# Optimization experiments

Measured on AMD Instinct MI355X. Metric: run time of the kernel, lower is better.

Reference implementation:

```python
import jax, jax.numpy as jnp
import numpy as np

B, D, H = 512, 256, 512

def setup_inputs() -> dict:
    key = jax.random.key(0)
    ks = jax.random.split(key, 7)
    s = lambda fan_in: 1.0 / np.sqrt(fan_in)
    return {
        "h": jax.random.normal(ks[0], (B, D), jnp.float32),
        "W1": jax.random.normal(ks[1], (2 * D, H), jnp.float32) * s(2 * D),
        "b1": jax.random.normal(ks[2], (H,), jnp.float32) * s(2 * D),
        "W2": jax.random.normal(ks[3], (H, H), jnp.float32) * s(H),
        "b2": jax.random.normal(ks[4], (H,), jnp.float32) * s(H),
        "W3": jax.random.normal(ks[5], (H, 1), jnp.float32) * s(H),
        "b3": jax.random.normal(ks[6], (1,), jnp.float32) * s(H),
    }

def reference(h, W1, b1, W2, b2, W3, b3):
    n = h.shape[0]
    # Split W1 into halves acting on hi and hj; equivalent to cat([hi,hj]) @ W1
    yi = h @ W1[:D]            # [B, H]
    yj = h @ W1[D:]            # [B, H]
    x = jnp.tanh(yi[:, None, :] + yj[None, :, :] + b1)   # [B, B, H]
    x = jnp.tanh(x @ W2 + b2)                             # [B, B, H]
    logits = (x @ W3 + b3)[..., 0]                        # [B, B]
    eye = jnp.eye(n, dtype=logits.dtype)
    return logits * (1.0 - eye) + (-20.0) * eye
```

## Files before the change

kernel.cpp:

```cpp
#include <hip/hip_runtime.h>
#include <cstdint>


#define NB 512
#define ND 256
#define NH 512
#define C2 2.885390081777927f

typedef int i32x4 __attribute__((ext_vector_type(4)));
typedef int i32x16 __attribute__((ext_vector_type(16)));
typedef unsigned int u32;
typedef unsigned char u8;

__device__ __forceinline__ float exp2_fast(float x) {
#if __has_builtin(__builtin_amdgcn_exp2f)
  return __builtin_amdgcn_exp2f(x);
#else
  return exp2f(x);
#endif
}
__device__ __forceinline__ float rcp_fast(float x) {
#if __has_builtin(__builtin_amdgcn_rcpf)
  return __builtin_amdgcn_rcpf(x);
#else
  return 1.0f / x;
#endif
}
__device__ __forceinline__ u32 perm_b32(u32 hi, u32 lo, u32 sel) {
#if __has_builtin(__builtin_amdgcn_perm)
  return __builtin_amdgcn_perm(hi, lo, sel);
#else
  u32 r = 0;
  for (int b = 0; b < 4; ++b) {
    const u32 c = (sel >> (8 * b)) & 255;
    const u32 byte = (c < 4) ? (lo >> (8 * c)) & 255 : (c < 8) ? (hi >> (8 * (c - 4))) & 255 : 0;
    r |= byte << (8 * b);
  }
  return r;
#endif
}

__global__ __launch_bounds__(256) void prep_all(const float* __restrict__ h,
                                                const float* __restrict__ W1,
                                                const float* __restrict__ b1,
                                                const float* __restrict__ W2,
                                                float* __restrict__ Ai,
                                                float* __restrict__ Aj,
                                                u8* __restrict__ W2q) {
  const int t = threadIdx.x;
  const int bx = blockIdx.x;
  if (bx < 256) {
    __shared__ float hsh[4][ND];
    const int i0 = (bx >> 1) * 4;
    const int n = (bx & 1) * 256 + t;
#pragma unroll
    for (int ii = 0; ii < 4; ++ii) hsh[ii][t] = h[(i0 + ii) * ND + t];
    __syncthreads();
    float ai[4] = {0.0f, 0.0f, 0.0f, 0.0f};
    float aj[4] = {0.0f, 0.0f, 0.0f, 0.0f};
#pragma unroll 4
    for (int d = 0; d < ND; ++d) {
      const float wa = W1[d * NH + n];
      const float wb = W1[(d + ND) * NH + n];
#pragma unroll
      for (int ii = 0; ii < 4; ++ii) {
        const float hd = hsh[ii][d];
        ai[ii] = fmaf(hd, wa, ai[ii]);
        aj[ii] = fmaf(hd, wb, aj[ii]);
      }
    }
    const float b1n = b1[n];
#pragma unroll
    for (int ii = 0; ii < 4; ++ii) {
      Ai[(i0 + ii) * NH + n] = ai[ii] * C2;
      Aj[(i0 + ii) * NH + n] = (aj[ii] + b1n) * C2;
    }
  } else {
    const int g = (bx - 256) * 256 + t;
    const int lane = g & 63;
    const int nt = (g >> 6) & 15;
    const int ks = g >> 10;
    const int n = nt * 32 + (lane & 31);
    const int kb = ks * 32 + ((lane >> 5) << 4);
    u32 w[4];
#pragma unroll
    for (int q = 0; q < 4; ++q) {
      u32 acc = 0;
#pragma unroll
      for (int j = 0; j < 4; ++j) {
        const float wv = fminf(fmaxf(W2[(kb + q * 4 + j) * NH + n], -0.25f), 0.25f);
        const int qi = (int)rintf(wv * 508.0f);
        acc |= ((u32)(qi & 255)) << (8 * j);
      }
      w[q] = acc;
    }
    ((uint4*)W2q)[g] = make_uint4(w[0], w[1], w[2], w[3]);
  }
}

__global__ __launch_bounds__(512, 4) void pair_main(const float* __restrict__ Ai,
                                                    const float* __restrict__ Aj,
                                                    const u8* __restrict__ W2q,
                                                    const float* __restrict__ b2,
                                                    const float* __restrict__ W3,
                                                    const float* __restrict__ b3,
                                                    float* __restrict__ out) {
  __shared__ __align__(16) u8 xs[32 * 512];
  __shared__ float red2[32][64];
  __shared__ float wsum[8];

  const int t = threadIdx.x;
  const int w = t >> 6;
  const int lane = t & 63;
  const int lhi = lane >> 5;
  const int llo = lane & 31;
  const int bx = blockIdx.x;
  const int i = bx >> 4;
  const int j0 = (bx & 15) * 32;

  const float SCALE = (0.25f / (127.0f * 127.0f)) * C2;
  float b2c[2], w3v[2];
#pragma unroll
  for (int ntl = 0; ntl < 2; ++ntl) {
    const int n = w * 64 + ntl * 32 + llo;
    b2c[ntl] = b2[n] * C2;
    w3v[ntl] = W3[n];
  }
  {
    float w3s = w3v[0] + w3v[1];
#pragma unroll
    for (int off = 1; off < 32; off <<= 1) w3s += __shfl_xor(w3s, off, 64);
    if (lane == 0) wsum[w] = w3s;
  }

  {
    const int srow = t & 31;
    const int ss0 = t >> 5;
    const int k0 = ss0 * 16;
    const float* ajr = Aj + (size_t)(j0 + srow) * NH;
    const float* air = Ai + (size_t)i * NH;
    float s[32];
#pragma unroll
    for (int g = 0; g < 8; ++g) {
      const int ko = k0 + (g & 3) * 4 + (g >> 2) * 256;
      const float4 fa = *(const float4*)(ajr + ko);
      const float4 ga = *(const float4*)(air + ko);
      s[g * 4 + 0] = fa.x + ga.x;
      s[g * 4 + 1] = fa.y + ga.y;
      s[g * 4 + 2] = fa.z + ga.z;
      s[g * 4 + 3] = fa.w + ga.w;
    }
#pragma unroll
    for (int q = 0; q < 32; ++q) s[q] = exp2_fast(s[q]);
#pragma unroll
    for (int q = 0; q < 32; ++q) s[q] = rcp_fast(s[q] + 1.0f);
    u32 m[32];
#pragma unroll
    for (int q = 0; q < 32; ++q) m[q] = __builtin_bit_cast(u32, fmaf(-254.0f, s[q], 12583039.0f));
    u32 wd[8];
#pragma unroll
    for (int g = 0; g < 8; ++g) {
      const u32 p01 = perm_b32(m[g * 4 + 1], m[g * 4 + 0], 0x0C0C0400u);
      const u32 p23 = perm_b32(m[g * 4 + 3], m[g * 4 + 2], 0x0C0C0400u);
      wd[g] = perm_b32(p23, p01, 0x05040100u);
    }
    ((uint4*)xs)[ss0 * 32 + srow] = make_uint4(wd[0], wd[1], wd[2], wd[3]);
    ((uint4*)xs)[(ss0 + 16) * 32 + srow] = make_uint4(wd[4], wd[5], wd[6], wd[7]);
  }
  __syncthreads();

  i32x16 acc[2];
#pragma unroll
  for (int nt = 0; nt < 2; ++nt)
#pragma unroll
    for (int q = 0; q < 16; ++q) acc[nt][q] = 0;

  const i32x4* xsv = (const i32x4*)xs;
  const int abase = lhi * 32 + llo;
  const uint4* w2v = (const uint4*)W2q + w * 128 + lane;

  i32x4 aP0 = xsv[abase];
  i32x4 aP1 = xsv[64 + abase];
  uint4 bP00 = w2v[0], bP01 = w2v[64];
  uint4 bP10 = w2v[1024], bP11 = w2v[1024 + 64];

#pragma unroll
  for (int kk = 0; kk < 8; ++kk) {
    const int ks0 = 2 * kk;
    {
      const i32x4 a = aP0;
      const i32x4 c0 = __builtin_bit_cast(i32x4, bP00);
      const i32x4 c1 = __builtin_bit_cast(i32x4, bP01);
      if (kk < 7) {
        aP0 = xsv[(ks0 + 2) * 64 + abase];
        const uint4* wp = w2v + (ks0 + 2) * 1024;
        bP00 = wp[0];
        bP01 = wp[64];
      }
      acc[0] = __builtin_amdgcn_mfma_i32_32x32x32_i8(a, c0, acc[0], 0, 0, 0);
      acc[1] = __builtin_amdgcn_mfma_i32_32x32x32_i8(a, c1, acc[1], 0, 0, 0);
    }
    {
      const i32x4 a = aP1;
      const i32x4 c0 = __builtin_bit_cast(i32x4, bP10);
      const i32x4 c1 = __builtin_bit_cast(i32x4, bP11);
      if (kk < 7) {
        aP1 = xsv[(ks0 + 3) * 64 + abase];
        const uint4* wp = w2v + (ks0 + 3) * 1024;
        bP10 = wp[0];
        bP11 = wp[64];
      }
      acc[0] = __builtin_amdgcn_mfma_i32_32x32x32_i8(a, c0, acc[0], 0, 0, 0);
      acc[1] = __builtin_amdgcn_mfma_i32_32x32x32_i8(a, c1, acc[1], 0, 0, 0);
    }
  }

  float ev[32];
#pragma unroll
  for (int reg = 0; reg < 16; ++reg) {
    ev[reg] = fmaf((float)acc[0][reg], SCALE, b2c[0]);
    ev[16 + reg] = fmaf((float)acc[1][reg], SCALE, b2c[1]);
  }
#pragma unroll
  for (int q = 0; q < 32; ++q) ev[q] = exp2_fast(ev[q]);
#pragma unroll
  for (int q = 0; q < 32; ++q) ev[q] = rcp_fast(ev[q] + 1.0f);

#pragma unroll
  for (int reg = 0; reg < 16; ++reg) {
    float sr = fmaf(w3v[0], ev[reg], w3v[1] * ev[16 + reg]);
    sr += __shfl_xor(sr, 1, 64);
    sr += __shfl_xor(sr, 2, 64);
    const int row = (reg & 3) + 8 * (reg >> 2) + 4 * lhi;
    if ((llo & 3) == 0) red2[row][w * 8 + (llo >> 2)] = sr;
  }
  __syncthreads();

  {
    const float w3tot = b3[0] + ((wsum[0] + wsum[1]) + (wsum[2] + wsum[3])) +
                        ((wsum[4] + wsum[5]) + (wsum[6] + wsum[7]));
    const int row = t >> 4;
    const int sub = t & 15;
    const float4 v = *(const float4*)&red2[row][sub * 4];
    float s2 = (v.x + v.y) + (v.z + v.w);
    s2 += __shfl_xor(s2, 1, 16);
    s2 += __shfl_xor(s2, 2, 16);
    s2 += __shfl_xor(s2, 4, 16);
    s2 += __shfl_xor(s2, 8, 16);
    if (sub == 0) {
      const int j = j0 + row;
      out[i * NB + j] = (j == i) ? -20.0f : fmaf(-2.0f, s2, w3tot);
    }
  }
}

extern "C" void kernel_launch(void* const* d_in, const int* in_sizes, int n_in,
                              void* d_out, int out_size, void* d_ws, size_t ws_size,
                              hipStream_t stream) {
  const float* h = (const float*)d_in[0];
  const float* W1 = (const float*)d_in[1];
  const float* b1 = (const float*)d_in[2];
  const float* W2 = (const float*)d_in[3];
  const float* b2 = (const float*)d_in[4];
  const float* W3 = (const float*)d_in[5];
  const float* b3 = (const float*)d_in[6];
  float* out = (float*)d_out;

  float* Ai = (float*)d_ws;
  float* Aj = Ai + NB * NH;
  u8* W2q = (u8*)(Aj + NB * NH);

  prep_all<<<320, 256, 0, stream>>>(h, W1, b1, W2, Ai, Aj, W2q);
  pair_main<<<8192, 512, 0, stream>>>(Ai, Aj, W2q, b2, W3, b3, out);
}
```

Baseline: 246.0 us.

## Replace tanh transcendentals with LDS lookup tables and retile W1 projection

Both tanh activations now use 2048-entry lookup tables instead of per-element exp2 and reciprocal. The tables are built by two extra blocks in the prep kernel and copied into shared memory by every pair_main block. The first table is stored twice to spread byte-lookup bank conflicts across lanes. The aim is to take work off the transcendental units in the pair kernel. In exchange it adds per-block table loads from global memory, an extra barrier and more LDS use. The W1 projection in prep is also retiled to stage h and W1 tiles through shared memory.

```diff
diff --git a/kernel.cpp b/kernel.cpp
--- a/kernel.cpp
+++ b/kernel.cpp
@@ -6,6 +6,13 @@
 #define ND 256
 #define NH 512
 #define C2 2.885390081777927f
+
+#define L1_X0 (-9.6f)
+#define L1_S (2048.0f / 19.2f)
+#define L1_IS (19.2f / 2048.0f)
+#define L2_Y0 (-12.0f)
+#define L2_S (2048.0f / 24.0f)
+#define L2_IS (24.0f / 2048.0f)
 
 typedef int i32x4 __attribute__((ext_vector_type(4)));
 typedef int i32x16 __attribute__((ext_vector_type(16)));
@@ -39,6 +46,10 @@
   return r;
 #endif
 }
+__device__ __forceinline__ u32 tanh_q127_magic(float u) {
+  const float r = rcp_fast(exp2_fast(u) + 1.0f);
+  return __builtin_bit_cast(u32, fmaf(-254.0f, r, 12583039.0f));
+}
 
 __global__ __launch_bounds__(256) void prep_all(const float* __restrict__ h,
                                                 const float* __restrict__ W1,
@@ -46,36 +57,75 @@
                                                 const float* __restrict__ W2,
                                                 float* __restrict__ Ai,
                                                 float* __restrict__ Aj,
-                                                u8* __restrict__ W2q) {
+                                                u8* __restrict__ W2q,
+                                                u8* __restrict__ lut1g,
+                                                float* __restrict__ lut2g) {
   const int t = threadIdx.x;
   const int bx = blockIdx.x;
   if (bx < 256) {
-    __shared__ float hsh[4][ND];
-    const int i0 = (bx >> 1) * 4;
-    const int n = (bx & 1) * 256 + t;
-#pragma unroll
-    for (int ii = 0; ii < 4; ++ii) hsh[ii][t] = h[(i0 + ii) * ND + t];
-    __syncthreads();
-    float ai[4] = {0.0f, 0.0f, 0.0f, 0.0f};
-    float aj[4] = {0.0f, 0.0f, 0.0f, 0.0f};
+    __shared__ float hs[32][68];
+    __shared__ float w1t[64][36];
+    __shared__ float w1b[64][36];
+    const int it = bx >> 4, nt = bx & 15;
+    const int i0 = it * 32, n0 = nt * 32;
+    const int nn = t & 31, ig = t >> 5;
+    float accA[4] = {0.f, 0.f, 0.f, 0.f}, accB[4] = {0.f, 0.f, 0.f, 0.f};
+    for (int c2 = 0; c2 < 4; ++c2) {
+      __syncthreads();
+      {
+        const int r = t >> 3, c0 = (t & 7) * 8;
+        const float* src = h + (size_t)(i0 + r) * ND + c2 * 64 + c0;
+        const float4 a = *(const float4*)src;
+        const float4 b = *(const float4*)(src + 4);
+        *(float4*)&hs[r][c0] = a;
+        *(float4*)&hs[r][c0 + 4] = b;
+      }
+      {
+        const int r = t >> 2, c0 = (t & 3) * 8;
+        const float* st = W1 + (size_t)(c2 * 64 + r) * NH + n0 + c0;
+        const float* sb = W1 + (size_t)(256 + c2 * 64 + r) * NH + n0 + c0;
+        const float4 a = *(const float4*)st;
+        const float4 b = *(const float4*)(st + 4);
+        const float4 c = *(const float4*)sb;
+        const float4 d = *(const float4*)(sb + 4);
+        *(float4*)&w1t[r][c0] = a;
+        *(float4*)&w1t[r][c0 + 4] = b;
+        *(float4*)&w1b[r][c0] = c;
+        *(float4*)&w1b[r][c0 + 4] = d;
+      }
+      __syncthreads();
 #pragma unroll 4
-    for (int d = 0; d < ND; ++d) {
-      const float wa = W1[d * NH + n];
-      const float wb = W1[(d + ND) * NH + n];
-#pragma unroll
-      for (int ii = 0; ii < 4; ++ii) {
-        const float hd = hsh[ii][d];
-        ai[ii] = fmaf(hd, wa, ai[ii]);
-        aj[ii] = fmaf(hd, wb, aj[ii]);
-      }
-    }
-    const float b1n = b1[n];
-#pragma unroll
-    for (int ii = 0; ii < 4; ++ii) {
-      Ai[(i0 + ii) * NH + n] = ai[ii] * C2;
-      Aj[(i0 + ii) * NH + n] = (aj[ii] + b1n) * C2;
-    }
-  } else {
+      for (int k4 = 0; k4 < 16; ++k4) {
+        const float4 hv0 = *(const float4*)&hs[ig * 4 + 0][k4 * 4];
+        const float4 hv1 = *(const float4*)&hs[ig * 4 + 1][k4 * 4];
+        const float4 hv2 = *(const float4*)&hs[ig * 4 + 2][k4 * 4];
+        const float4 hv3 = *(const float4*)&hs[ig * 4 + 3][k4 * 4];
+        const float* h0 = (const float*)&hv0;
+        const float* h1 = (const float*)&hv1;
+        const float* h2 = (const float*)&hv2;
+        const float* h3 = (const float*)&hv3;
+#pragma unroll
+        for (int j = 0; j < 4; ++j) {
+          const float wtj = w1t[k4 * 4 + j][nn];
+          const float wbj = w1b[k4 * 4 + j][nn];
+          accA[0] = fmaf(h0[j], wtj, accA[0]);
+          accA[1] = fmaf(h1[j], wtj, accA[1]);
+          accA[2] = fmaf(h2[j], wtj, accA[2]);
+          accA[3] = fmaf(h3[j], wtj, accA[3]);
+          accB[0] = fmaf(h0[j], wbj, accB[0]);
+          accB[1] = fmaf(h1[j], wbj, accB[1]);
+          accB[2] = fmaf(h2[j], wbj, accB[2]);
+          accB[3] = fmaf(h3[j], wbj, accB[3]);
+        }
+      }
+    }
+    const float b1n = b1[n0 + nn];
+#pragma unroll
+    for (int r = 0; r < 4; ++r) {
+      Ai[(size_t)(i0 + ig * 4 + r) * NH + n0 + nn] = accA[r] * C2;
+      Aj[(size_t)(i0 + ig * 4 + r) * NH + n0 + nn] = (accB[r] + b1n) * C2;
+    }
+  } else if (bx < 320) {
     const int g = (bx - 256) * 256 + t;
     const int lane = g & 63;
     const int nt = (g >> 6) & 15;
@@ -95,6 +145,20 @@
       w[q] = acc;
     }
     ((uint4*)W2q)[g] = make_uint4(w[0], w[1], w[2], w[3]);
+  } else if (bx == 320) {
+#pragma unroll
+    for (int r = 0; r < 8; ++r) {
+      const int e = t + r * 256;
+      const float u = fmaf((float)e, L1_IS, L1_X0);
+      lut1g[e] = (u8)(tanh_q127_magic(u) & 255u);
+    }
+  } else {
+#pragma unroll
+    for (int r = 0; r < 8; ++r) {
+      const int e = t + r * 256;
+      const float u = fmaf((float)e, L2_IS, L2_Y0);
+      lut2g[e] = rcp_fast(exp2_fast(u) + 1.0f);
+    }
   }
 }
 
@@ -104,8 +168,12 @@
                                                     const float* __restrict__ b2,
                                                     const float* __restrict__ W3,
                                                     const float* __restrict__ b3,
+                                                    const u8* __restrict__ lut1g,
+                                                    const float* __restrict__ lut2g,
                                                     float* __restrict__ out) {
   __shared__ __align__(16) u8 xs[32 * 512];
+  __shared__ __align__(16) u8 lut1[4096];
+  __shared__ __align__(16) float lut2[2048];
   __shared__ float red2[32][64];
   __shared__ float wsum[8];
 
@@ -118,12 +186,24 @@
   const int i = bx >> 4;
   const int j0 = (bx & 15) * 32;
 
+  if (t < 128) {
+    const uint4 v = ((const uint4*)lut1g)[t];
+    ((uint4*)lut1)[t] = v;
+    ((uint4*)lut1)[128 + t] = v;
+  }
+  {
+    const uint4 v2 = ((const uint4*)lut2g)[t];
+    ((uint4*)lut2)[t] = v2;
+  }
+
   const float SCALE = (0.25f / (127.0f * 127.0f)) * C2;
-  float b2c[2], w3v[2];
+  const float K1 = SCALE * L2_S;
+  const float O2 = 0.5f - L2_Y0 * L2_S;
+  float K2[2], w3v[2];
 #pragma unroll
   for (int ntl = 0; ntl < 2; ++ntl) {
     const int n = w * 64 + ntl * 32 + llo;
-    b2c[ntl] = b2[n] * C2;
+    K2[ntl] = fmaf(b2[n] * C2, L2_S, O2);
     w3v[ntl] = W3[n];
   }
   {
@@ -132,6 +212,7 @@
     for (int off = 1; off < 32; off <<= 1) w3s += __shfl_xor(w3s, off, 64);
     if (lane == 0) wsum[w] = w3s;
   }
+  __syncthreads();
 
   {
     const int srow = t & 31;
@@ -139,33 +220,30 @@
     const int k0 = ss0 * 16;
     const float* ajr = Aj + (size_t)(j0 + srow) * NH;
     const float* air = Ai + (size_t)i * NH;
-    float s[32];
-#pragma unroll
-    for (int g = 0; g < 8; ++g) {
-      const int ko = k0 + (g & 3) * 4 + (g >> 2) * 256;
-      const float4 fa = *(const float4*)(ajr + ko);
-      const float4 ga = *(const float4*)(air + ko);
-      s[g * 4 + 0] = fa.x + ga.x;
-      s[g * 4 + 1] = fa.y + ga.y;
-      s[g * 4 + 2] = fa.z + ga.z;
-      s[g * 4 + 3] = fa.w + ga.w;
-    }
-#pragma unroll
-    for (int q = 0; q < 32; ++q) s[q] = exp2_fast(s[q]);
-#pragma unroll
-    for (int q = 0; q < 32; ++q) s[q] = rcp_fast(s[q] + 1.0f);
-    u32 m[32];
-#pragma unroll
-    for (int q = 0; q < 32; ++q) m[q] = __builtin_bit_cast(u32, fmaf(-254.0f, s[q], 12583039.0f));
-    u32 wd[8];
-#pragma unroll
-    for (int g = 0; g < 8; ++g) {
-      const u32 p01 = perm_b32(m[g * 4 + 1], m[g * 4 + 0], 0x0C0C0400u);
-      const u32 p23 = perm_b32(m[g * 4 + 3], m[g * 4 + 2], 0x0C0C0400u);
-      wd[g] = perm_b32(p23, p01, 0x05040100u);
-    }
-    ((uint4*)xs)[ss0 * 32 + srow] = make_uint4(wd[0], wd[1], wd[2], wd[3]);
-    ((uint4*)xs)[(ss0 + 16) * 32 + srow] = make_uint4(wd[4], wd[5], wd[6], wd[7]);
+    const u8* lp = lut1 + ((lane & 1) << 11);
+    const float O1 = 0.5f - L1_X0 * L1_S;
+#pragma unroll
+    for (int uu = 0; uu < 2; ++uu) {
+      const int koff = k0 + uu * 256;
+      u32 wd[4];
+#pragma unroll
+      for (int q = 0; q < 4; ++q) {
+        const float4 fa = *(const float4*)(ajr + koff + q * 4);
+        const float4 ga = *(const float4*)(air + koff + q * 4);
+        float us[4] = {fa.x + ga.x, fa.y + ga.y, fa.z + ga.z, fa.w + ga.w};
+        u32 m[4];
+#pragma unroll
+        for (int e = 0; e < 4; ++e) {
+          float f = fmaf(us[e], L1_S, O1);
+          f = fminf(fmaxf(f, 0.0f), 2047.0f);
+          m[e] = lp[(u32)f];
+        }
+        const u32 p01 = perm_b32(m[1], m[0], 0x0C0C0400u);
+        const u32 p23 = perm_b32(m[3], m[2], 0x0C0C0400u);
+        wd[q] = perm_b32(p23, p01, 0x05040100u);
+      }
+      ((uint4*)xs)[(ss0 + uu * 16) * 32 + srow] = make_uint4(wd[0], wd[1], wd[2], wd[3]);
+    }
   }
   __syncthreads();
 
@@ -215,20 +293,15 @@
     }
   }
 
-  float ev[32];
 #pragma unroll
   for (int reg = 0; reg < 16; ++reg) {
-    ev[reg] = fmaf((float)acc[0][reg], SCALE, b2c[0]);
-    ev[16 + reg] = fmaf((float)acc[1][reg], SCALE, b2c[1]);
-  }
-#pragma unroll
-  for (int q = 0; q < 32; ++q) ev[q] = exp2_fast(ev[q]);
-#pragma unroll
-  for (int q = 0; q < 32; ++q) ev[q] = rcp_fast(ev[q] + 1.0f);
-
-#pragma unroll
-  for (int reg = 0; reg < 16; ++reg) {
-    float sr = fmaf(w3v[0], ev[reg], w3v[1] * ev[16 + reg]);
+    float f0 = fmaf((float)acc[0][reg], K1, K2[0]);
+    float f1 = fmaf((float)acc[1][reg], K1, K2[1]);
+    f0 = fminf(fmaxf(f0, 0.0f), 2047.0f);
+    f1 = fminf(fmaxf(f1, 0.0f), 2047.0f);
+    const float r0 = lut2[(u32)f0];
+    const float r1 = lut2[(u32)f1];
+    float sr = fmaf(w3v[0], r0, w3v[1] * r1);
     sr += __shfl_xor(sr, 1, 64);
     sr += __shfl_xor(sr, 2, 64);
     const int row = (reg & 3) + 8 * (reg >> 2) + 4 * lhi;
@@ -269,7 +342,9 @@
   float* Ai = (float*)d_ws;
   float* Aj = Ai + NB * NH;
   u8* W2q = (u8*)(Aj + NB * NH);
-
-  prep_all<<<320, 256, 0, stream>>>(h, W1, b1, W2, Ai, Aj, W2q);
-  pair_main<<<8192, 512, 0, stream>>>(Ai, Aj, W2q, b2, W3, b3, out);
-}
+  u8* lut1g = W2q + NB * NH;
+  float* lut2g = (float*)(lut1g + 2048);
+
+  prep_all<<<322, 256, 0, stream>>>(h, W1, b1, W2, Ai, Aj, W2q, lut1g, lut2g);
+  pair_main<<<8192, 512, 0, stream>>>(Ai, Aj, W2q, b2, W3, b3, lut1g, lut2g, out);
+}
```

Result: no change. 242.1 us (-1.6%).
